# Kernel optimization log

Hardware: AMD Instinct MI355X
Metric: run time of the kernel (lower is better)

Reference implementation:

```python
import jax, jax.numpy as jnp
import numpy as np

CH3 = np.array([[0,1,2],[1,2,3],[2,3,4],[3,4,5],[0,4,5],[0,1,5]])  # [6,3]
CH4 = np.array([[0,1,2,3],[1,2,3,4],[2,3,4,5],[0,3,4,5],[0,1,4,5],
                [0,1,2,5],[0,1,3,4],[1,2,4,5],[0,2,3,5]])          # [9,4]
K = 5

def setup_inputs() -> dict:
    key = jax.random.key(0)
    ks = jax.random.split(key, 8)
    x  = jax.random.normal(ks[0], (32, 6, 512, 512), dtype=jnp.float32)
    # params, scaled like torch default kaiming-uniform-ish (bound = 1/sqrt(fan_in))
    def u(k, shape, fan_in):
        b = 1.0 / np.sqrt(fan_in)
        return jax.random.uniform(k, shape, jnp.float32, -b, b)
    w3 = u(ks[1], (6, 3, K, K), 3 * K * K)
    b3 = u(ks[2], (6,), 3 * K * K)
    w4 = u(ks[3], (9, 4, K, K), 4 * K * K)
    b4 = u(ks[4], (9,), 4 * K * K)
    w6 = u(ks[5], (1, 6, K, K), 6 * K * K)
    b6 = u(ks[6], (1,), 6 * K * K)
    return {"x": x, "w3": w3, "b3": b3, "w4": w4, "b4": b4, "w6": w6, "b6": b6}

def _full_kernel(w3, w4, w6):
    # Scatter the per-subset filters into one [16,6,5,5] OIHW kernel; unused
    # input channels stay zero, which is mathematically identical to gathering
    # channel subsets per the original module.
    W = jnp.zeros((16, 6, K, K), dtype=w3.dtype)
    W = W.at[jnp.arange(6)[:, None], CH3].set(w3)
    W = W.at[(6 + jnp.arange(9))[:, None], CH4].set(w4)
    W = W.at[15].set(w6[0])
    return W

def reference(x, w3, b3, w4, b4, w6, b6):
    Wfull = _full_kernel(w3, w4, w6)
    bias = jnp.concatenate([b3, b4, b6])  # [16]
    out = jax.lax.conv_general_dilated(
        x, Wfull, window_strides=(1, 1), padding='VALID',
        dimension_numbers=('NCHW', 'OIHW', 'NCHW'))
    return out + bias[None, :, None, None]  # [B,16,H-4,W-4]
```

## Files before the change

kernel.cpp:

```cpp
#include <hip/hip_runtime.h>


#define OW 508
#define BX 64
#define BY 16
#define TC 68
#define TR 21
#define TPAD 4

typedef _Float16 h8 __attribute__((ext_vector_type(8)));
typedef _Float16 h2 __attribute__((ext_vector_type(2)));
typedef float f32x4 __attribute__((ext_vector_type(4)));

__device__ __constant__ int d_CH3[6][3] = {
    {0,1,2},{1,2,3},{2,3,4},{3,4,5},{0,4,5},{0,1,5}};
__device__ __constant__ int d_CH4[9][4] = {
    {0,1,2,3},{1,2,3,4},{2,3,4,5},{0,3,4,5},{0,1,4,5},
    {0,1,2,5},{0,1,3,4},{1,2,4,5},{0,2,3,5}};

__global__ void prep_weights(const float* __restrict__ w3, const float* __restrict__ b3,
                             const float* __restrict__ w4, const float* __restrict__ b4,
                             const float* __restrict__ w6, const float* __restrict__ b6,
                             float* __restrict__ bias, unsigned short* __restrict__ AF) {
    __shared__ float Wfull[16 * 6 * 25];
    const int tid = threadIdx.x;
    for (int i = tid; i < 16 * 6 * 25; i += 256) Wfull[i] = 0.f;
    __syncthreads();
    for (int i = tid; i < 6 * 3 * 25; i += 256) {
        int oc = i / 75, r = i % 75, c = r / 25, t = r % 25;
        Wfull[(oc * 6 + d_CH3[oc][c]) * 25 + t] = w3[i];
    }
    for (int i = tid; i < 9 * 4 * 25; i += 256) {
        int o = i / 100, r = i % 100, c = r / 25, t = r % 25;
        Wfull[((6 + o) * 6 + d_CH4[o][c]) * 25 + t] = w4[i];
    }
    for (int i = tid; i < 6 * 25; i += 256) Wfull[15 * 150 + i] = w6[i];
    __syncthreads();
    for (int i = tid; i < 5 * 2 * 64 * 8; i += 256) {
        int e = i & 7, lane = (i >> 3) & 63, ch = (i >> 9) & 1, kx = i >> 10;
        int oc = lane & 15, ky = ch * 4 + (lane >> 4);
        float w = 0.f;
        if (ky < 5 && e < 6) w = Wfull[(oc * 6 + e) * 25 + ky * 5 + kx];
        _Float16 hw = (_Float16)w;
        AF[i] = __builtin_bit_cast(unsigned short, hw);
    }
    if (tid < 6)        bias[tid] = b3[tid];
    else if (tid < 15)  bias[tid] = b4[tid - 6];
    else if (tid == 15) bias[tid] = b6[0];
}

__global__ __launch_bounds__(256) void conv_mfma(
        const float* __restrict__ x, const unsigned short* __restrict__ AF,
        const float* __restrict__ bias, float* __restrict__ out) {
    __shared__ uint4 T4[TC * TR + TPAD];

    const int tid = threadIdx.x;
    const int gx0 = blockIdx.x * BX;
    const int oy0 = blockIdx.y * BY;
    const int bz  = blockIdx.z;
    const float* xb = x + (size_t)bz * 6 * 512 * 512;

    unsigned int* Tw = (unsigned int*)T4;
    for (int idx = tid; idx < TC * TR * 4 + TPAD * 4; idx += 256) {
        unsigned int val = 0u;
        int waddr = idx;
        if (idx < TC * TR * 4) {
            int c  = idx % TC;
            int rr = (idx / TC) % TR;
            int ip = idx / (TC * TR);
            waddr = c * 84 + rr * 4 + ip;
            int gy = oy0 + rr, gx = gx0 + c;
            if (ip < 3 && rr < 20 && gy < 512 && gx < 512) {
                const float* p0 = xb + ((size_t)(2 * ip) * 512 + gy) * 512 + gx;
                float v0 = p0[0];
                float v1 = p0[262144];
                h2 h; h.x = (_Float16)v0; h.y = (_Float16)v1;
                val = __builtin_bit_cast(unsigned int, h);
            }
        }
        Tw[waddr] = val;
    }
    __syncthreads();

    const int lane = tid & 63;
    const int n = lane & 15;
    const int g = lane >> 4;

    h8 afr[10];
    #pragma unroll
    for (int q = 0; q < 10; ++q)
        afr[q] = *reinterpret_cast<const h8*>(AF + (q * 64 + lane) * 8);

    f32x4 binit;
    binit.x = bias[g * 4 + 0];
    binit.y = bias[g * 4 + 1];
    binit.z = bias[g * 4 + 2];
    binit.w = bias[g * 4 + 3];

    const int wstrip = tid >> 6;
    const int col0   = wstrip * 16;
    const int px     = gx0 + col0 + n;
    const int tbase  = (col0 + n) * TR + g;

    #pragma unroll 1
    for (int d = 0; d < BY; ++d) {
        f32x4 acc = binit;
        #pragma unroll
        for (int kx = 0; kx < 5; ++kx) {
            #pragma unroll
            for (int ch = 0; ch < 2; ++ch) {
                h8 b = *reinterpret_cast<const h8*>(&T4[tbase + kx * TR + ch * 4 + d]);
                acc = __builtin_amdgcn_mfma_f32_16x16x32_f16(afr[kx * 2 + ch], b, acc, 0, 0, 0);
            }
        }
        const int oy = oy0 + d;
        if (oy < OW && px < OW) {
            size_t o0 = (((size_t)bz * 16 + g * 4) * OW + oy) * OW + px;
            const size_t cs = (size_t)OW * OW;
            out[o0]          = acc.x;
            out[o0 + cs]     = acc.y;
            out[o0 + 2 * cs] = acc.z;
            out[o0 + 3 * cs] = acc.w;
        }
    }
}

extern "C" void kernel_launch(void* const* d_in, const int* in_sizes, int n_in,
                              void* d_out, int out_size, void* d_ws, size_t ws_size,
                              hipStream_t stream) {
    const float* x  = (const float*)d_in[0];
    const float* w3 = (const float*)d_in[1];
    const float* b3 = (const float*)d_in[2];
    const float* w4 = (const float*)d_in[3];
    const float* b4 = (const float*)d_in[4];
    const float* w6 = (const float*)d_in[5];
    const float* b6 = (const float*)d_in[6];
    float* out = (float*)d_out;

    float* bias        = (float*)d_ws;
    unsigned short* AF = (unsigned short*)(bias + 16);

    prep_weights<<<1, 256, 0, stream>>>(w3, b3, w4, b4, w6, b6, bias, AF);

    dim3 grid((OW + BX - 1) / BX, (OW + BY - 1) / BY, 32);
    conv_mfma<<<grid, 256, 0, stream>>>(x, AF, bias, out);
}
```

Measured before the change: 267.4 us.

## Fully unroll row loop with register reuse of LDS B fragments and nontemporal stores

The 16-row output loop is fully unrolled into four groups of four rows. The B fragments loaded from LDS are kept in two ping-pong register arrays, so the second-half fragment of one row is reused as the first-half fragment of the row four below. This roughly halves LDS reads per MFMA and lets loads overlap compute. Output stores become nontemporal to avoid polluting cache. The cost is higher register pressure from 40 h8 fragments, which may reduce occupancy.

```diff
diff --git a/kernel.cpp b/kernel.cpp
--- a/kernel.cpp
+++ b/kernel.cpp
@@ -47,6 +47,37 @@
     if (tid < 6)        bias[tid] = b3[tid];
     else if (tid < 15)  bias[tid] = b4[tid - 6];
     else if (tid == 15) bias[tid] = b6[0];
+}
+
+template<int T>
+__device__ __forceinline__ void conv_group(const uint4* __restrict__ Tb,
+        const h8 (&afr)[10], const h8 (&cur)[5][4], h8 (&nxt)[5][4],
+        f32x4 binit, float* __restrict__ out, size_t o00, int oy0, int px) {
+    #pragma unroll
+    for (int kx = 0; kx < 5; ++kx)
+        #pragma unroll
+        for (int i = 0; i < 4; ++i)
+            nxt[kx][i] = *reinterpret_cast<const h8*>(&Tb[kx * TR + 4 * T + 4 + i]);
+
+    #pragma unroll
+    for (int i = 0; i < 4; ++i) {
+        const int d = 4 * T + i;
+        f32x4 acc = binit;
+        #pragma unroll
+        for (int kx = 0; kx < 5; ++kx) {
+            acc = __builtin_amdgcn_mfma_f32_16x16x32_f16(afr[2 * kx + 0], cur[kx][i], acc, 0, 0, 0);
+            acc = __builtin_amdgcn_mfma_f32_16x16x32_f16(afr[2 * kx + 1], nxt[kx][i], acc, 0, 0, 0);
+        }
+        const int oy = oy0 + d;
+        if (oy < OW && px < OW) {
+            const size_t cs = (size_t)OW * OW;
+            size_t o0 = o00 + (size_t)d * OW;
+            __builtin_nontemporal_store(acc.x, &out[o0]);
+            __builtin_nontemporal_store(acc.y, &out[o0 + cs]);
+            __builtin_nontemporal_store(acc.z, &out[o0 + 2 * cs]);
+            __builtin_nontemporal_store(acc.w, &out[o0 + 3 * cs]);
+        }
+    }
 }
 
 __global__ __launch_bounds__(256) void conv_mfma(
@@ -100,29 +131,21 @@
     const int wstrip = tid >> 6;
     const int col0   = wstrip * 16;
     const int px     = gx0 + col0 + n;
-    const int tbase  = (col0 + n) * TR + g;
+    const uint4* Tb  = &T4[(col0 + n) * TR + g];
 
-    #pragma unroll 1
-    for (int d = 0; d < BY; ++d) {
-        f32x4 acc = binit;
+    const size_t o00 = (((size_t)bz * 16 + g * 4) * OW + oy0) * OW + px;
+
+    h8 BE[5][4], BO[5][4];
+    #pragma unroll
+    for (int kx = 0; kx < 5; ++kx)
         #pragma unroll
-        for (int kx = 0; kx < 5; ++kx) {
-            #pragma unroll
-            for (int ch = 0; ch < 2; ++ch) {
-                h8 b = *reinterpret_cast<const h8*>(&T4[tbase + kx * TR + ch * 4 + d]);
-                acc = __builtin_amdgcn_mfma_f32_16x16x32_f16(afr[kx * 2 + ch], b, acc, 0, 0, 0);
-            }
-        }
-        const int oy = oy0 + d;
-        if (oy < OW && px < OW) {
-            size_t o0 = (((size_t)bz * 16 + g * 4) * OW + oy) * OW + px;
-            const size_t cs = (size_t)OW * OW;
-            out[o0]          = acc.x;
-            out[o0 + cs]     = acc.y;
-            out[o0 + 2 * cs] = acc.z;
-            out[o0 + 3 * cs] = acc.w;
-        }
-    }
+        for (int i = 0; i < 4; ++i)
+            BE[kx][i] = *reinterpret_cast<const h8*>(&Tb[kx * TR + i]);
+
+    conv_group<0>(Tb, afr, BE, BO, binit, out, o00, oy0, px);
+    conv_group<1>(Tb, afr, BO, BE, binit, out, o00, oy0, px);
+    conv_group<2>(Tb, afr, BE, BO, binit, out, o00, oy0, px);
+    conv_group<3>(Tb, afr, BO, BE, binit, out, o00, oy0, px);
 }
 
 extern "C" void kernel_launch(void* const* d_in, const int* in_sizes, int n_in,
```

Measured after the change: 422.6 us. 1.58x slower.

## Switch conv to 32x32x16 MFMA computing two output rows per pass

Applied to the files above, without the earlier changes.

The convolution now uses 32x32x16 f16 MFMA instead of 16x16x32. The 32-row M dimension packs 16 output channels times 2 output rows, and the weight fragments are rebuilt with ky offsets so that three K-chunks per kx cover both rows. The block width doubles to 128 columns and each wave handles 32 pixel columns. This cuts MFMA issue count and redundant shared-memory B loads per output, and larger tiles lower halo overhead. In exchange it uses more LDS and accumulator registers, and outputs are written as 8 scattered channel stores per row.

```diff
diff --git a/kernel.cpp b/kernel.cpp
--- a/kernel.cpp
+++ b/kernel.cpp
@@ -2,15 +2,14 @@
 
 
 #define OW 508
-#define BX 64
+#define BX 128
 #define BY 16
-#define TC 68
+#define TC 132
 #define TR 21
-#define TPAD 4
 
 typedef _Float16 h8 __attribute__((ext_vector_type(8)));
 typedef _Float16 h2 __attribute__((ext_vector_type(2)));
-typedef float f32x4 __attribute__((ext_vector_type(4)));
+typedef float f32x16 __attribute__((ext_vector_type(16)));
 
 __device__ __constant__ int d_CH3[6][3] = {
     {0,1,2},{1,2,3},{2,3,4},{3,4,5},{0,4,5},{0,1,5}};
@@ -36,11 +35,13 @@
     }
     for (int i = tid; i < 6 * 25; i += 256) Wfull[15 * 150 + i] = w6[i];
     __syncthreads();
-    for (int i = tid; i < 5 * 2 * 64 * 8; i += 256) {
-        int e = i & 7, lane = (i >> 3) & 63, ch = (i >> 9) & 1, kx = i >> 10;
-        int oc = lane & 15, ky = ch * 4 + (lane >> 4);
+    for (int i = tid; i < 15 * 64 * 8; i += 256) {
+        int e = i & 7, lane = (i >> 3) & 63, q = i >> 9;
+        int kx = q / 3, ch = q % 3;
+        int oc = lane & 15, dy = (lane >> 4) & 1, rr = lane >> 5;
+        int ky = ch * 2 + rr - dy;
         float w = 0.f;
-        if (ky < 5 && e < 6) w = Wfull[(oc * 6 + e) * 25 + ky * 5 + kx];
+        if (e < 6 && ky >= 0 && ky <= 4) w = Wfull[(oc * 6 + e) * 25 + ky * 5 + kx];
         _Float16 hw = (_Float16)w;
         AF[i] = __builtin_bit_cast(unsigned short, hw);
     }
@@ -52,7 +53,7 @@
 __global__ __launch_bounds__(256) void conv_mfma(
         const float* __restrict__ x, const unsigned short* __restrict__ AF,
         const float* __restrict__ bias, float* __restrict__ out) {
-    __shared__ uint4 T4[TC * TR + TPAD];
+    __shared__ uint4 T4[TC * TR];
 
     const int tid = threadIdx.x;
     const int gx0 = blockIdx.x * BX;
@@ -61,66 +62,69 @@
     const float* xb = x + (size_t)bz * 6 * 512 * 512;
 
     unsigned int* Tw = (unsigned int*)T4;
-    for (int idx = tid; idx < TC * TR * 4 + TPAD * 4; idx += 256) {
+    for (int idx = tid; idx < TC * TR * 4; idx += 256) {
+        int c  = idx % TC;
+        int rr = (idx / TC) % TR;
+        int ip = idx / (TC * TR);
+        int waddr = c * (TR * 4) + rr * 4 + ip;
         unsigned int val = 0u;
-        int waddr = idx;
-        if (idx < TC * TR * 4) {
-            int c  = idx % TC;
-            int rr = (idx / TC) % TR;
-            int ip = idx / (TC * TR);
-            waddr = c * 84 + rr * 4 + ip;
-            int gy = oy0 + rr, gx = gx0 + c;
-            if (ip < 3 && rr < 20 && gy < 512 && gx < 512) {
-                const float* p0 = xb + ((size_t)(2 * ip) * 512 + gy) * 512 + gx;
-                float v0 = p0[0];
-                float v1 = p0[262144];
-                h2 h; h.x = (_Float16)v0; h.y = (_Float16)v1;
-                val = __builtin_bit_cast(unsigned int, h);
-            }
+        int gy = oy0 + rr, gx = gx0 + c;
+        if (ip < 3 && rr < 20 && gy < 512 && gx < 512) {
+            const float* p0 = xb + ((size_t)(2 * ip) * 512 + gy) * 512 + gx;
+            float v0 = p0[0];
+            float v1 = p0[262144];
+            h2 h; h.x = (_Float16)v0; h.y = (_Float16)v1;
+            val = __builtin_bit_cast(unsigned int, h);
         }
         Tw[waddr] = val;
     }
     __syncthreads();
 
     const int lane = tid & 63;
-    const int n = lane & 15;
-    const int g = lane >> 4;
+    const int n = lane & 31;
+    const int h = lane >> 5;
 
-    h8 afr[10];
+    h8 afr[15];
     #pragma unroll
-    for (int q = 0; q < 10; ++q)
+    for (int q = 0; q < 15; ++q)
         afr[q] = *reinterpret_cast<const h8*>(AF + (q * 64 + lane) * 8);
 
-    f32x4 binit;
-    binit.x = bias[g * 4 + 0];
-    binit.y = bias[g * 4 + 1];
-    binit.z = bias[g * 4 + 2];
-    binit.w = bias[g * 4 + 3];
+    f32x16 binit;
+    #pragma unroll
+    for (int reg = 0; reg < 16; ++reg)
+        binit[reg] = bias[((reg & 3) + 8 * ((reg >> 2) & 1) + 4 * h) & 15];
 
-    const int wstrip = tid >> 6;
-    const int col0   = wstrip * 16;
-    const int px     = gx0 + col0 + n;
-    const int tbase  = (col0 + n) * TR + g;
+    const int wv   = tid >> 6;
+    const int col0 = wv * 32;
+    const int px   = gx0 + col0 + n;
+    const uint4* Tb = &T4[(col0 + n) * TR + h];
+
+    const size_t cs = (size_t)OW * OW;
+    const bool px_ok = (px < OW);
+    float* ob = out + ((size_t)bz * 16 + 4 * h) * cs + px;
 
     #pragma unroll 1
-    for (int d = 0; d < BY; ++d) {
-        f32x4 acc = binit;
+    for (int d = 0; d < BY; d += 2) {
+        f32x16 acc = binit;
         #pragma unroll
         for (int kx = 0; kx < 5; ++kx) {
             #pragma unroll
-            for (int ch = 0; ch < 2; ++ch) {
-                h8 b = *reinterpret_cast<const h8*>(&T4[tbase + kx * TR + ch * 4 + d]);
-                acc = __builtin_amdgcn_mfma_f32_16x16x32_f16(afr[kx * 2 + ch], b, acc, 0, 0, 0);
+            for (int ch = 0; ch < 3; ++ch) {
+                h8 b = *reinterpret_cast<const h8*>(&Tb[kx * TR + d + ch * 2]);
+                acc = __builtin_amdgcn_mfma_f32_32x32x16_f16(afr[kx * 3 + ch], b, acc, 0, 0, 0);
             }
         }
-        const int oy = oy0 + d;
-        if (oy < OW && px < OW) {
-            size_t o0 = (((size_t)bz * 16 + g * 4) * OW + oy) * OW + px;
-            const size_t cs = (size_t)OW * OW;
-            out[o0]          = acc.x;
-            out[o0 + cs]     = acc.y;
-            out[o0 + 2 * cs] = acc.z;
-            out[o0 + 3 * cs] = acc.w;
+        #pragma unroll
+        for (int dy = 0; dy < 2; ++dy) {
+            const int oy = oy0 + d + dy;
+            if (oy < OW && px_ok) {
+                #pragma unroll
+                for (int reg8 = 0; reg8 < 8; ++reg8) {
+                    const int reg = dy * 8 + reg8;
+                    const int ocb = (reg & 3) + 8 * ((reg >> 2) & 1);
+                    ob[(size_t)ocb * cs + (size_t)oy * OW] = acc[reg];
+                }
+            }
         }
     }
 }
```

New measurement: 295.0 us. 1.1x slower.
